# Performance work log

Hardware: AMD Instinct MI355X
Metric: run time of the kernel (lower is better)

## Reference

```python
import jax, jax.numpy as jnp
import numpy as np
from math import sqrt

N_NODES = 50000
N_EDGES = 800000
NUM_RADIAL = 6
HIDDEN = 128
FACTOR2 = HIDDEN // 2  # factor*2 = hidden/2


def swish(v):
    return v * jax.nn.sigmoid(v)


def setup_inputs() -> dict:
    key = jax.random.key(0)
    ks = jax.random.split(key, 9)
    s3 = sqrt(3.0)
    x = jax.random.randint(ks[0], (N_NODES, 2), 0, 20, dtype=jnp.int64)
    rbf = jax.random.normal(ks[1], (N_EDGES, NUM_RADIAL), dtype=jnp.float32)
    i = jax.random.randint(ks[2], (N_EDGES,), 0, N_NODES, dtype=jnp.int64)
    j = jax.random.randint(ks[3], (N_EDGES,), 0, N_NODES, dtype=jnp.int64)
    resi_emb_w = jax.random.uniform(ks[4], (20, FACTOR2), jnp.float32, -s3, s3)
    atom_emb_w = jax.random.uniform(ks[5], (95, FACTOR2), jnp.float32, -s3, s3)
    # torch Linear default init: U(-1/sqrt(fan_in), 1/sqrt(fan_in))
    b1 = 1.0 / sqrt(NUM_RADIAL)
    W_rbf = jax.random.uniform(ks[6], (HIDDEN, NUM_RADIAL), jnp.float32, -b1, b1)
    b_rbf = jax.random.uniform(ks[7], (HIDDEN,), jnp.float32, -b1, b1)
    b2 = 1.0 / sqrt(3 * HIDDEN)
    kA, kB = jax.random.split(ks[8])
    W_lin = jax.random.uniform(kA, (HIDDEN, 3 * HIDDEN), jnp.float32, -b2, b2)
    b_lin = jax.random.uniform(kB, (HIDDEN,), jnp.float32, -b2, b2)
    return {"x": x, "rbf": rbf, "i": i, "j": j,
            "resi_emb_w": resi_emb_w, "atom_emb_w": atom_emb_w,
            "W_rbf": W_rbf, "b_rbf": b_rbf, "W_lin": W_lin, "b_lin": b_lin}


def reference(x, rbf, i, j, resi_emb_w, atom_emb_w, W_rbf, b_rbf, W_lin, b_lin):
    # node features: concat of residue and atom embeddings -> [N, hidden]
    node = jnp.concatenate([resi_emb_w[x[:, 0]], atom_emb_w[x[:, 1]]], axis=-1)
    # rbf projection + swish -> [E, hidden]
    rbf_h = swish(rbf @ W_rbf.T + b_rbf)
    # edge-wise gather + concat + linear + swish -> [E, hidden]
    h = jnp.concatenate([node[i], node[j], rbf_h], axis=-1)
    return swish(h @ W_lin.T + b_lin)
```

## Files before the change

### kernel.cpp

```cpp
#include <hip/hip_runtime.h>
#include <hip/hip_bf16.h>
#include <hip/hip_fp16.h>

typedef _Float16 f16x8  __attribute__((ext_vector_type(8)));
typedef __fp16   h16x2  __attribute__((ext_vector_type(2)));
typedef float    f32x4  __attribute__((ext_vector_type(4)));
typedef float    f32x16 __attribute__((ext_vector_type(16)));

#define KDIM     384
#define MBLK     64
#define PADK     392
#define NEDGE    800000
#define WP_ELEMS 49152

__device__ __forceinline__ float fast_swish(float v) {
  return v * __builtin_amdgcn_rcpf(1.0f + __expf(-v));
}

__device__ __forceinline__ void pack8(_Float16* dst, float4 a, float4 b) {
  union { h16x2 h[4]; f16x8 v; } u;
  u.h[0] = __builtin_amdgcn_cvt_pkrtz(a.x, a.y);
  u.h[1] = __builtin_amdgcn_cvt_pkrtz(a.z, a.w);
  u.h[2] = __builtin_amdgcn_cvt_pkrtz(b.x, b.y);
  u.h[3] = __builtin_amdgcn_cvt_pkrtz(b.z, b.w);
  *(f16x8*)dst = u.v;
}

__global__ void pack_w_kernel(const float* __restrict__ W_lin,
                              const float* __restrict__ W_rbf,
                              _Float16* __restrict__ Wp,
                              _Float16* __restrict__ Wrp) {
  int idx = blockIdx.x * 256 + threadIdx.x;
  if (idx < WP_ELEMS) {
    int e  = idx & 7;
    int l  = (idx >> 3) & 63;
    int nt = (idx >> 9) & 3;
    int ks = idx >> 11;
    int n  = nt * 32 + (l & 31);
    int k  = ks * 16 + ((l >> 5) << 3) + e;
    Wp[idx] = (_Float16)W_lin[n * KDIM + k];
  } else if (idx < WP_ELEMS + 4096) {
    int idx2 = idx - WP_ELEMS;
    int e  = idx2 & 7;
    int l  = (idx2 >> 3) & 63;
    int nt = idx2 >> 9;
    int k  = ((l >> 4) << 3) + e;
    float v = (k < 6) ? W_rbf[(nt * 16 + (l & 15)) * 6 + k] : 0.0f;
    Wrp[idx2] = (_Float16)v;
  }
}

__global__ __launch_bounds__(256, 3)
void embed_main_kernel(const int* __restrict__ x,
                       const float* __restrict__ rbf,
                       const int* __restrict__ gi,
                       const int* __restrict__ gj,
                       const float* __restrict__ resi_w,
                       const float* __restrict__ atom_w,
                       const float* __restrict__ b_rbf,
                       const float* __restrict__ b_lin,
                       const _Float16* __restrict__ Wp,
                       const _Float16* __restrict__ Wrp,
                       float* __restrict__ out) {
  __shared__ alignas(16) _Float16 hlds[MBLK][PADK];
  const int tid  = threadIdx.x;
  const int e0   = blockIdx.x * MBLK;
  const int lane = tid & 63;
  const int wave = tid >> 6;
  const int m    = wave >> 1;
  const int nb   = (wave & 1) * 2;
  const int c5   = lane & 31;
  const int g2   = lane >> 5;

  const f16x8* wp2 = (const f16x8*)Wp + lane;

  f16x8 breg[2][12];
  #pragma unroll
  for (int q = 0; q < 12; ++q) {
    int ks = q >> 1, ntg = nb + (q & 1);
    breg[0][q] = wp2[(ks * 4 + ntg) * 64];
  }

  const int cc  = tid & 15;
  const int seg = cc >> 2;
  const int off = (cc & 3) << 4;
  const int* __restrict__ gsel = (seg < 2) ? gi : gj;
  const float* __restrict__ tbl = (seg & 1) ? atom_w : resi_w;
  const int m0 = tid >> 4;
  int sel_[4];
  #pragma unroll
  for (int it = 0; it < 4; ++it) {
    int node = gsel[e0 + m0 + it * 16];
    sel_[it] = x[(node << 1) + (seg & 1)];
  }

  {
    const int g = lane >> 4;
    const int c = lane & 15;
    f16x8 ra = {0, 0, 0, 0, 0, 0, 0, 0};
    if (g == 0) {
      const float* rp = rbf + (size_t)(e0 + wave * 16 + c) * 6;
      ra[0] = (_Float16)rp[0]; ra[1] = (_Float16)rp[1]; ra[2] = (_Float16)rp[2];
      ra[3] = (_Float16)rp[3]; ra[4] = (_Float16)rp[4]; ra[5] = (_Float16)rp[5];
    }
    const f16x8* wrb = (const f16x8*)Wrp + lane;
    #pragma unroll
    for (int nt = 0; nt < 8; ++nt) {
      f16x8 rb = wrb[nt * 64];
      f32x4 d = __builtin_amdgcn_mfma_f32_16x16x32_f16(ra, rb,
                  (f32x4){0.f, 0.f, 0.f, 0.f}, 0, 0, 0);
      float bb = b_rbf[nt * 16 + c];
      #pragma unroll
      for (int r = 0; r < 4; ++r) {
        float vv = d[r] + bb;
        hlds[wave * 16 + 4 * g + r][256 + nt * 16 + c] = (_Float16)fast_swish(vv);
      }
    }
  }

  #pragma unroll
  for (int it = 0; it < 4; ++it) {
    int mm = m0 + it * 16;
    const float4* s4 = (const float4*)(tbl + sel_[it] * 64 + off);
    float4 v0 = s4[0], v1 = s4[1], v2 = s4[2], v3 = s4[3];
    _Float16* dst = &hlds[mm][cc << 4];
    pack8(dst,     v0, v1);
    pack8(dst + 8, v2, v3);
  }
  __syncthreads();

  const _Float16* abase = &hlds[(m << 5) + c5][g2 << 3];

  f32x16 acc0 = {};
  f32x16 acc1 = {};

  #pragma unroll
  for (int chunk = 0; chunk < 4; ++chunk) {
    if (chunk < 3) {
      #pragma unroll
      for (int q = 0; q < 12; ++q) {
        int ks = (chunk + 1) * 6 + (q >> 1), ntg = nb + (q & 1);
        breg[(chunk + 1) & 1][q] = wp2[(ks * 4 + ntg) * 64];
      }
    }
    #pragma unroll
    for (int kl = 0; kl < 6; ++kl) {
      int ks = chunk * 6 + kl;
      f16x8 a = *(const f16x8*)(abase + ks * 16);
      acc0 = __builtin_amdgcn_mfma_f32_32x32x16_f16(a, breg[chunk & 1][kl * 2],     acc0, 0, 0, 0);
      acc1 = __builtin_amdgcn_mfma_f32_32x32x16_f16(a, breg[chunk & 1][kl * 2 + 1], acc1, 0, 0, 0);
    }
  }

  const int colA = (wave & 1) * 64 + c5;
  const int colB = colA + 32;
  const float blA = b_lin[colA];
  const float blB = b_lin[colB];
  #pragma unroll
  for (int reg = 0; reg < 16; ++reg) {
    int row = (reg & 3) + 8 * (reg >> 2) + 4 * g2;
    float* orow = out + (size_t)(e0 + (m << 5) + row) * 128;
    orow[colA] = fast_swish(acc0[reg] + blA);
    orow[colB] = fast_swish(acc1[reg] + blB);
  }
}

extern "C" void kernel_launch(void* const* d_in, const int* in_sizes, int n_in,
                              void* d_out, int out_size, void* d_ws, size_t ws_size,
                              hipStream_t stream) {
  const int*   x      = (const int*)d_in[0];
  const float* rbf    = (const float*)d_in[1];
  const int*   gi     = (const int*)d_in[2];
  const int*   gj     = (const int*)d_in[3];
  const float* resi_w = (const float*)d_in[4];
  const float* atom_w = (const float*)d_in[5];
  const float* W_rbf  = (const float*)d_in[6];
  const float* b_rbf  = (const float*)d_in[7];
  const float* W_lin  = (const float*)d_in[8];
  const float* b_lin  = (const float*)d_in[9];
  float* out = (float*)d_out;
  _Float16* Wp  = (_Float16*)d_ws;
  _Float16* Wrp = (_Float16*)d_ws + WP_ELEMS;

  hipLaunchKernelGGL(pack_w_kernel, dim3(208), dim3(256), 0, stream,
                     W_lin, W_rbf, Wp, Wrp);
  hipLaunchKernelGGL(embed_main_kernel, dim3(NEDGE / MBLK), dim3(256), 0, stream,
                     x, rbf, gi, gj, resi_w, atom_w, b_rbf, b_lin, Wp, Wrp, out);
}
```

Measured before the change: 221.5 us.

## Precompute fp16 node table and load A fragments directly from global

A new prep kernel builds a packed fp16 node-feature table once per call. The main kernel then loads each edge's node_i and node_j rows straight into MFMA A-operand registers, so only the rbf part goes through LDS. This cuts the LDS footprint, which allows launch bounds of 4 blocks per SM, and removes the double-buffered B-register prefetch in favour of direct per-step weight loads. The costs are an extra kernel launch and a 12.8MB workspace write, and the A gathers are strided global reads with no reuse.

```diff
diff --git a/kernel.cpp b/kernel.cpp
--- a/kernel.cpp
+++ b/kernel.cpp
@@ -7,11 +7,13 @@
 typedef float    f32x4  __attribute__((ext_vector_type(4)));
 typedef float    f32x16 __attribute__((ext_vector_type(16)));
 
-#define KDIM     384
-#define MBLK     64
-#define PADK     392
-#define NEDGE    800000
-#define WP_ELEMS 49152
+#define KDIM       384
+#define MBLK       64
+#define NEDGE      800000
+#define NNODES     50000
+#define NODE_ELEMS (NNODES * 128)
+#define WP_ELEMS   49152
+#define HRPAD      136
 
 __device__ __forceinline__ float fast_swish(float v) {
   return v * __builtin_amdgcn_rcpf(1.0f + __expf(-v));
@@ -24,6 +26,20 @@
   u.h[2] = __builtin_amdgcn_cvt_pkrtz(b.x, b.y);
   u.h[3] = __builtin_amdgcn_cvt_pkrtz(b.z, b.w);
   *(f16x8*)dst = u.v;
+}
+
+__global__ void prep_node_kernel(const int* __restrict__ x,
+                                 const float* __restrict__ resi_w,
+                                 const float* __restrict__ atom_w,
+                                 _Float16* __restrict__ node) {
+  int idx = blockIdx.x * 256 + threadIdx.x;
+  int n = idx >> 4, cg = idx & 15;
+  int isAtom = cg >> 3;
+  int off = (cg & 7) << 3;
+  int sel = x[(n << 1) + isAtom];
+  const float4* s4 = (const float4*)((isAtom ? atom_w : resi_w) + sel * 64 + off);
+  float4 v0 = s4[0], v1 = s4[1];
+  pack8(node + n * 128 + cg * 8, v0, v1);
 }
 
 __global__ void pack_w_kernel(const float* __restrict__ W_lin,
@@ -50,19 +66,17 @@
   }
 }
 
-__global__ __launch_bounds__(256, 3)
-void embed_main_kernel(const int* __restrict__ x,
-                       const float* __restrict__ rbf,
+__global__ __launch_bounds__(256, 4)
+void embed_main_kernel(const float* __restrict__ rbf,
                        const int* __restrict__ gi,
                        const int* __restrict__ gj,
-                       const float* __restrict__ resi_w,
-                       const float* __restrict__ atom_w,
                        const float* __restrict__ b_rbf,
                        const float* __restrict__ b_lin,
+                       const _Float16* __restrict__ node,
                        const _Float16* __restrict__ Wp,
                        const _Float16* __restrict__ Wrp,
                        float* __restrict__ out) {
-  __shared__ alignas(16) _Float16 hlds[MBLK][PADK];
+  __shared__ alignas(16) _Float16 hr[MBLK][HRPAD];
   const int tid  = threadIdx.x;
   const int e0   = blockIdx.x * MBLK;
   const int lane = tid & 63;
@@ -72,27 +86,14 @@
   const int c5   = lane & 31;
   const int g2   = lane >> 5;
 
-  const f16x8* wp2 = (const f16x8*)Wp + lane;
-
-  f16x8 breg[2][12];
+  const int erow = e0 + (m << 5) + c5;
+  const int ni = gi[erow];
+  const int nj = gj[erow];
+  const f16x8* Ai = (const f16x8*)(node + ni * 128) + g2;
+  const f16x8* Aj = (const f16x8*)(node + nj * 128) + g2;
+  f16x8 ai[8], aj[8];
   #pragma unroll
-  for (int q = 0; q < 12; ++q) {
-    int ks = q >> 1, ntg = nb + (q & 1);
-    breg[0][q] = wp2[(ks * 4 + ntg) * 64];
-  }
-
-  const int cc  = tid & 15;
-  const int seg = cc >> 2;
-  const int off = (cc & 3) << 4;
-  const int* __restrict__ gsel = (seg < 2) ? gi : gj;
-  const float* __restrict__ tbl = (seg & 1) ? atom_w : resi_w;
-  const int m0 = tid >> 4;
-  int sel_[4];
-  #pragma unroll
-  for (int it = 0; it < 4; ++it) {
-    int node = gsel[e0 + m0 + it * 16];
-    sel_[it] = x[(node << 1) + (seg & 1)];
-  }
+  for (int k = 0; k < 8; ++k) { ai[k] = Ai[2 * k]; aj[k] = Aj[2 * k]; }
 
   {
     const int g = lane >> 4;
@@ -113,43 +114,34 @@
       #pragma unroll
       for (int r = 0; r < 4; ++r) {
         float vv = d[r] + bb;
-        hlds[wave * 16 + 4 * g + r][256 + nt * 16 + c] = (_Float16)fast_swish(vv);
+        hr[wave * 16 + 4 * g + r][nt * 16 + c] = (_Float16)fast_swish(vv);
       }
     }
   }
-
-  #pragma unroll
-  for (int it = 0; it < 4; ++it) {
-    int mm = m0 + it * 16;
-    const float4* s4 = (const float4*)(tbl + sel_[it] * 64 + off);
-    float4 v0 = s4[0], v1 = s4[1], v2 = s4[2], v3 = s4[3];
-    _Float16* dst = &hlds[mm][cc << 4];
-    pack8(dst,     v0, v1);
-    pack8(dst + 8, v2, v3);
-  }
   __syncthreads();
 
-  const _Float16* abase = &hlds[(m << 5) + c5][g2 << 3];
-
+  const f16x8* wp2 = (const f16x8*)Wp + lane;
   f32x16 acc0 = {};
   f32x16 acc1 = {};
 
   #pragma unroll
-  for (int chunk = 0; chunk < 4; ++chunk) {
-    if (chunk < 3) {
-      #pragma unroll
-      for (int q = 0; q < 12; ++q) {
-        int ks = (chunk + 1) * 6 + (q >> 1), ntg = nb + (q & 1);
-        breg[(chunk + 1) & 1][q] = wp2[(ks * 4 + ntg) * 64];
-      }
-    }
-    #pragma unroll
-    for (int kl = 0; kl < 6; ++kl) {
-      int ks = chunk * 6 + kl;
-      f16x8 a = *(const f16x8*)(abase + ks * 16);
-      acc0 = __builtin_amdgcn_mfma_f32_32x32x16_f16(a, breg[chunk & 1][kl * 2],     acc0, 0, 0, 0);
-      acc1 = __builtin_amdgcn_mfma_f32_32x32x16_f16(a, breg[chunk & 1][kl * 2 + 1], acc1, 0, 0, 0);
-    }
+  for (int ks = 0; ks < 8; ++ks) {
+    f16x8 a = ai[ks];
+    acc0 = __builtin_amdgcn_mfma_f32_32x32x16_f16(a, wp2[(ks * 4 + nb) * 64],     acc0, 0, 0, 0);
+    acc1 = __builtin_amdgcn_mfma_f32_32x32x16_f16(a, wp2[(ks * 4 + nb + 1) * 64], acc1, 0, 0, 0);
+  }
+  #pragma unroll
+  for (int ks = 8; ks < 16; ++ks) {
+    f16x8 a = aj[ks - 8];
+    acc0 = __builtin_amdgcn_mfma_f32_32x32x16_f16(a, wp2[(ks * 4 + nb) * 64],     acc0, 0, 0, 0);
+    acc1 = __builtin_amdgcn_mfma_f32_32x32x16_f16(a, wp2[(ks * 4 + nb + 1) * 64], acc1, 0, 0, 0);
+  }
+  const _Float16* hbase = &hr[(m << 5) + c5][g2 << 3];
+  #pragma unroll
+  for (int ks = 16; ks < 24; ++ks) {
+    f16x8 a = *(const f16x8*)(hbase + (ks - 16) * 16);
+    acc0 = __builtin_amdgcn_mfma_f32_32x32x16_f16(a, wp2[(ks * 4 + nb) * 64],     acc0, 0, 0, 0);
+    acc1 = __builtin_amdgcn_mfma_f32_32x32x16_f16(a, wp2[(ks * 4 + nb + 1) * 64], acc1, 0, 0, 0);
   }
 
   const int colA = (wave & 1) * 64 + c5;
@@ -179,11 +171,15 @@
   const float* W_lin  = (const float*)d_in[8];
   const float* b_lin  = (const float*)d_in[9];
   float* out = (float*)d_out;
-  _Float16* Wp  = (_Float16*)d_ws;
-  _Float16* Wrp = (_Float16*)d_ws + WP_ELEMS;
 
+  _Float16* node = (_Float16*)d_ws;
+  _Float16* Wp   = (_Float16*)d_ws + NODE_ELEMS;
+  _Float16* Wrp  = (_Float16*)d_ws + NODE_ELEMS + WP_ELEMS;
+
+  hipLaunchKernelGGL(prep_node_kernel, dim3(NNODES * 16 / 256), dim3(256), 0, stream,
+                     x, resi_w, atom_w, node);
   hipLaunchKernelGGL(pack_w_kernel, dim3(208), dim3(256), 0, stream,
                      W_lin, W_rbf, Wp, Wrp);
   hipLaunchKernelGGL(embed_main_kernel, dim3(NEDGE / MBLK), dim3(256), 0, stream,
-                     x, rbf, gi, gj, resi_w, atom_w, b_rbf, b_lin, Wp, Wrp, out);
+                     rbf, gi, gj, b_rbf, b_lin, node, Wp, Wrp, out);
 }
```

Measured after the change: 259.7 us. 17.2% more time.
